# Optimization experiments

Hardware: AMD Instinct MI355X
Metric: run time of the kernel (lower is better)

## Reference

```python
import jax, jax.numpy as jnp
import numpy as np

D_MODEL = 1024
N_HEADS = 16
D_HEAD = 64
GROUP_SIZE = 2
N_GROUPS = N_HEADS // GROUP_SIZE


def setup_inputs() -> dict:
    key = jax.random.key(0)
    k1, k2, k3, k4, k5 = jax.random.split(key, 5)
    def xavier(k, shape):
        fan_in, fan_out = shape[0], int(np.prod(shape[1:]))
        bound = float(np.sqrt(6.0 / (fan_in + fan_out)))
        return jax.random.uniform(k, shape, jnp.float32, -bound, bound)
    return {
        'resid': jax.random.normal(k1, (2, 2048, D_MODEL), jnp.float32),
        'W_Q': xavier(k2, (D_MODEL, N_HEADS, D_HEAD)),
        'W_K': xavier(k3, (D_MODEL, N_GROUPS, D_HEAD)),
        'W_V': xavier(k4, (D_MODEL, N_GROUPS, D_HEAD)),
        'W_out': xavier(k5, (D_HEAD, N_HEADS, D_MODEL)),
        'b_out': jnp.zeros((D_MODEL,), jnp.float32),
    }


def reference(resid, W_Q, W_K, W_V, W_out, b_out):
    batch, seq, _ = resid.shape
    # q: [b, s, n_heads, d_head] -> [b, s, n_groups, group_size, d_head]
    q = jnp.einsum('bsd,dhe->bshe', resid, W_Q)
    q = q.reshape(batch, seq, N_GROUPS, GROUP_SIZE, D_HEAD)
    k = jnp.einsum('bsd,dge->bsge', resid, W_K)  # [b, s, g, e]
    v = jnp.einsum('bsd,dge->bsge', resid, W_V)
    # scores: [b, g, group_size, qseq, kseq]
    scores = jnp.einsum('bqgre,bkge->bgrqk', q, k) / jnp.sqrt(jnp.float32(D_HEAD))
    causal_mask = jnp.triu(jnp.ones((seq, seq), bool), k=1)
    scores = jnp.where(causal_mask, jnp.float32(-1000000.0), scores)
    probs = jax.nn.softmax(scores, axis=-1)
    # z: [b, q, g, r, e]
    z = jnp.einsum('bgrqk,bkge->bqgre', probs, v)
    z = z.reshape(batch, seq, N_HEADS, D_HEAD)
    out = jnp.einsum('bshe,ehd->bsd', z, W_out) + b_out
    return out
```

## Files before the change

### kernel.cpp

```cpp
#include <hip/hip_runtime.h>

#define BATCH   2
#define SEQ     2048
#define DMODEL  1024
#define NHEADS  16
#define DHEAD   64
#define NGROUPS 8
#define NTOK    (BATCH * SEQ)
#define QKV_N   2048

typedef unsigned short ushort_t;
typedef unsigned int u32;
typedef __attribute__((ext_vector_type(8))) short short8;
typedef __attribute__((ext_vector_type(4))) float f32x4;
typedef __attribute__((ext_vector_type(16))) float f32x16;

#define MFMA16(a, b, c) __builtin_amdgcn_mfma_f32_16x16x32_bf16((a), (b), (c), 0, 0, 0)
#define MFMA32(a, b, c) __builtin_amdgcn_mfma_f32_32x32x16_bf16((a), (b), (c), 0, 0, 0)

#define GLOAD16(gp, lp)                                                        \
    __builtin_amdgcn_global_load_lds(                                          \
        (const u32 __attribute__((address_space(1)))*)(gp),                    \
        (u32 __attribute__((address_space(3)))*)(lp), 16, 0, 0)

#define CVTPK(dst, lo, hi) \
    asm("v_cvt_pk_bf16_f32 %0, %1, %2" : "=v"(dst) : "v"(lo), "v"(hi))

#define PLSWAP(a, b) \
    asm("v_permlane32_swap_b32 %0, %1" : "+v"(a), "+v"(b))

__device__ __forceinline__ ushort_t f2bu(float x) {
    unsigned u = __builtin_bit_cast(unsigned, x);
    unsigned r = (u + 0x7fffu + ((u >> 16) & 1u)) >> 16;
    return (ushort_t)r;
}

__global__ __launch_bounds__(256) void prep(
    const float* __restrict__ resid,
    const float* __restrict__ Wq, const float* __restrict__ Wk,
    const float* __restrict__ Wv, const float* __restrict__ Wout,
    ushort_t* __restrict__ rbf, ushort_t* __restrict__ Wt,
    ushort_t* __restrict__ Wot)
{
    __shared__ float Ws[64][65];
    const int t = threadIdx.x;
    const int bid = blockIdx.x;

    if (bid < 4096) {
        const int i4 = bid * 256 + t;
        union { float4 v; float f[4]; } a;
        a.v = *reinterpret_cast<const float4*>(resid + (size_t)i4 * 4);
        union { uint2 v; ushort_t u[4]; } o;
        #pragma unroll
        for (int j = 0; j < 4; ++j) o.u[j] = f2bu(a.f[j]);
        *reinterpret_cast<uint2*>(rbf + (size_t)i4 * 4) = o.v;
        return;
    }

    if (bid < 4096 + 512) {
        const int rel = bid - 4096;
        const int k0 = (rel & 15) * 64;
        const int n0 = (rel >> 4) * 64;

        const float* src; int stride, boff;
        if (n0 < 1024)       { src = Wq; stride = 1024; boff = n0; }
        else if (n0 < 1536)  { src = Wk; stride = 512;  boff = n0 - 1024; }
        else                 { src = Wv; stride = 512;  boff = n0 - 1536; }

        #pragma unroll
        for (int i = 0; i < 4; ++i) {
            const int c = i * 256 + t;
            const int row = c >> 4, cc = (c & 15) * 4;
            union { float4 v; float f[4]; } a;
            a.v = *reinterpret_cast<const float4*>(
                src + (size_t)(k0 + row) * stride + boff + cc);
            #pragma unroll
            for (int j = 0; j < 4; ++j) Ws[row][cc + j] = a.f[j];
        }
        __syncthreads();
        #pragma unroll
        for (int i = 0; i < 2; ++i) {
            const int c = i * 256 + t;
            const int nr = c >> 3, kc = (c & 7) * 8;
            union { uint4 v; ushort_t u[8]; } o;
            #pragma unroll
            for (int j = 0; j < 8; ++j) o.u[j] = f2bu(Ws[kc + j][nr]);
            *reinterpret_cast<uint4*>(Wt + (size_t)(n0 + nr) * 1024 + k0 + kc) = o.v;
        }
        return;
    }

    {
        const int rel = bid - 4608;
        const int d0 = (rel & 15) * 64;
        const int h  = rel >> 4;

        #pragma unroll
        for (int i = 0; i < 4; ++i) {
            const int c = i * 256 + t;
            const int e = c >> 4, dd = (c & 15) * 4;
            union { float4 v; float f[4]; } a;
            a.v = *reinterpret_cast<const float4*>(
                Wout + (size_t)(e * 16 + h) * 1024 + d0 + dd);
            #pragma unroll
            for (int j = 0; j < 4; ++j) Ws[e][dd + j] = a.f[j];
        }
        __syncthreads();
        #pragma unroll
        for (int i = 0; i < 2; ++i) {
            const int c = i * 256 + t;
            const int dr = c >> 3, ec = (c & 7) * 8;
            union { uint4 v; ushort_t u[8]; } o;
            #pragma unroll
            for (int j = 0; j < 8; ++j) o.u[j] = f2bu(Ws[ec + j][dr]);
            *reinterpret_cast<uint4*>(Wot + (size_t)(d0 + dr) * 1024 + h * 64 + ec) = o.v;
        }
    }
}

__global__ __launch_bounds__(256) void tr_v(
    const ushort_t* __restrict__ qkv, ushort_t* __restrict__ Vt)
{
    __shared__ ushort_t T[64][72];
    const int t  = threadIdx.x;
    const int s0 = blockIdx.x * 64;
    const int g  = blockIdx.y;
    const int b  = blockIdx.z;

    #pragma unroll
    for (int i = 0; i < 2; ++i) {
        const int c = i * 256 + t;
        const int row = c >> 3, ec = (c & 7) * 8;
        *reinterpret_cast<uint4*>(&T[row][ec]) =
            *reinterpret_cast<const uint4*>(
                qkv + (size_t)(b * SEQ + s0 + row) * QKV_N + 1536 + g * 64 + ec);
    }
    __syncthreads();
    #pragma unroll
    for (int i = 0; i < 2; ++i) {
        const int c = i * 256 + t;
        const int er = c >> 3, sc = (c & 7) * 8;
        union { uint4 v; ushort_t u[8]; } o;
        #pragma unroll
        for (int j = 0; j < 8; ++j) o.u[j] = T[sc + j][er];
        *reinterpret_cast<uint4*>(
            Vt + (size_t)((b * NGROUPS + g) * 64 + er) * SEQ + s0 + sc) = o.v;
    }
}

__global__ __launch_bounds__(512) void qkv_gemm(
    const ushort_t* __restrict__ A, const ushort_t* __restrict__ Bt,
    ushort_t* __restrict__ C)
{
    __shared__ ushort_t As[2][128][64];
    __shared__ ushort_t Bs[2][128][64];

    const int t = threadIdx.x;
    const int wave = t >> 6, lane = t & 63;
    const int quad = lane >> 4, x = lane & 15;
    const int wm = (wave >> 1) * 32, wn = (wave & 1) * 64;
    const int m0 = blockIdx.y * 128, n0 = blockIdx.x * 128;

    const int sr8 = lane >> 3;
    const int gc  = (lane & 7) ^ sr8;

    f32x4 acc[2][4];
    #pragma unroll
    for (int i = 0; i < 2; ++i)
        #pragma unroll
        for (int j = 0; j < 4; ++j) acc[i][j] = (f32x4)(0.f);

    #pragma unroll
    for (int s = 0; s < 2; ++s) {
        const int r0 = (wave * 2 + s) * 8;
        GLOAD16(A  + (size_t)(m0 + r0 + sr8) * 1024 + gc * 8, &As[0][r0][0]);
        GLOAD16(Bt + (size_t)(n0 + r0 + sr8) * 1024 + gc * 8, &Bs[0][r0][0]);
    }
    __syncthreads();

    int cur = 0;
    for (int k0 = 0; k0 < 1024; k0 += 64) {
        if (k0 + 64 < 1024) {
            #pragma unroll
            for (int s = 0; s < 2; ++s) {
                const int r0 = (wave * 2 + s) * 8;
                GLOAD16(A  + (size_t)(m0 + r0 + sr8) * 1024 + k0 + 64 + gc * 8,
                        &As[cur ^ 1][r0][0]);
                GLOAD16(Bt + (size_t)(n0 + r0 + sr8) * 1024 + k0 + 64 + gc * 8,
                        &Bs[cur ^ 1][r0][0]);
            }
        }
        #pragma unroll
        for (int j = 0; j < 2; ++j) {
            const int cs = ((j * 4 + quad) ^ (x & 7)) * 8;
            short8 af[2], bf[4];
            #pragma unroll
            for (int mt = 0; mt < 2; ++mt)
                af[mt] = *reinterpret_cast<const short8*>(&As[cur][wm + mt * 16 + x][cs]);
            #pragma unroll
            for (int nt = 0; nt < 4; ++nt)
                bf[nt] = *reinterpret_cast<const short8*>(&Bs[cur][wn + nt * 16 + x][cs]);
            #pragma unroll
            for (int mt = 0; mt < 2; ++mt)
                #pragma unroll
                for (int nt = 0; nt < 4; ++nt)
                    acc[mt][nt] = MFMA16(af[mt], bf[nt], acc[mt][nt]);
        }
        __syncthreads();
        cur ^= 1;
    }

    #pragma unroll
    for (int mt = 0; mt < 2; ++mt)
        #pragma unroll
        for (int nt = 0; nt < 4; ++nt)
            #pragma unroll
            for (int r = 0; r < 4; ++r) {
                const int row = m0 + wm + mt * 16 + quad * 4 + r;
                const int col = n0 + wn + nt * 16 + x;
                C[(size_t)row * QKV_N + col] = f2bu(acc[mt][nt][r]);
            }
}

__global__ __launch_bounds__(512) void out_gemm(
    const ushort_t* __restrict__ A, const ushort_t* __restrict__ Bt,
    const float* __restrict__ bias, float* __restrict__ C)
{
    __shared__ ushort_t As[2][128][64];
    __shared__ ushort_t Bs[2][64][64];

    const int t = threadIdx.x;
    const int wave = t >> 6, lane = t & 63;
    const int quad = lane >> 4, x = lane & 15;
    const int wm = (wave >> 1) * 32, wn = (wave & 1) * 32;
    const int m0 = blockIdx.y * 128, n0 = blockIdx.x * 64;

    const int sr8 = lane >> 3;
    const int gc  = (lane & 7) ^ sr8;

    f32x4 acc[2][2];
    #pragma unroll
    for (int i = 0; i < 2; ++i)
        #pragma unroll
        for (int j = 0; j < 2; ++j) acc[i][j] = (f32x4)(0.f);

    #pragma unroll
    for (int s = 0; s < 2; ++s) {
        const int r0 = (wave * 2 + s) * 8;
        GLOAD16(A + (size_t)(m0 + r0 + sr8) * 1024 + gc * 8, &As[0][r0][0]);
    }
    {
        const int r0 = wave * 8;
        GLOAD16(Bt + (size_t)(n0 + r0 + sr8) * 1024 + gc * 8, &Bs[0][r0][0]);
    }
    __syncthreads();

    int cur = 0;
    for (int k0 = 0; k0 < 1024; k0 += 64) {
        if (k0 + 64 < 1024) {
            #pragma unroll
            for (int s = 0; s < 2; ++s) {
                const int r0 = (wave * 2 + s) * 8;
                GLOAD16(A + (size_t)(m0 + r0 + sr8) * 1024 + k0 + 64 + gc * 8,
                        &As[cur ^ 1][r0][0]);
            }
            const int r0 = wave * 8;
            GLOAD16(Bt + (size_t)(n0 + r0 + sr8) * 1024 + k0 + 64 + gc * 8,
                    &Bs[cur ^ 1][r0][0]);
        }
        #pragma unroll
        for (int j = 0; j < 2; ++j) {
            const int cs = ((j * 4 + quad) ^ (x & 7)) * 8;
            short8 af[2], bf[2];
            #pragma unroll
            for (int mt = 0; mt < 2; ++mt)
                af[mt] = *reinterpret_cast<const short8*>(&As[cur][wm + mt * 16 + x][cs]);
            #pragma unroll
            for (int nt = 0; nt < 2; ++nt)
                bf[nt] = *reinterpret_cast<const short8*>(&Bs[cur][wn + nt * 16 + x][cs]);
            #pragma unroll
            for (int mt = 0; mt < 2; ++mt)
                #pragma unroll
                for (int nt = 0; nt < 2; ++nt)
                    acc[mt][nt] = MFMA16(af[mt], bf[nt], acc[mt][nt]);
        }
        __syncthreads();
        cur ^= 1;
    }

    float bv[2];
    #pragma unroll
    for (int nt = 0; nt < 2; ++nt) bv[nt] = bias[n0 + wn + nt * 16 + x];

    #pragma unroll
    for (int mt = 0; mt < 2; ++mt)
        #pragma unroll
        for (int nt = 0; nt < 2; ++nt)
            #pragma unroll
            for (int r = 0; r < 4; ++r) {
                const int row = m0 + wm + mt * 16 + quad * 4 + r;
                const int col = n0 + wn + nt * 16 + x;
                C[(size_t)row * 1024 + col] = acc[mt][nt][r] + bv[nt];
            }
}

__global__ __launch_bounds__(512, 4) void attn(
    const ushort_t* __restrict__ qkv, const ushort_t* __restrict__ Vt,
    ushort_t* __restrict__ z)
{
    __shared__ float Ob1[64 * 64];
    __shared__ float Ob3[64 * 64];
    __shared__ float Ofin[64 * 64];
    __shared__ float Lb1[64];
    __shared__ float Lb3[64];

    const int t = threadIdx.x;
    const int wave = t >> 6, lane = t & 63;
    const int x31 = lane & 31, hi = lane >> 5;
    const int rw = wave & 1;
    const int kw = wave >> 1;

    const int h  = blockIdx.x;
    const int qp = blockIdx.y;
    const int b  = blockIdx.z;
    const int g  = h >> 1;

    const ushort_t* kg = qkv + (size_t)(b * SEQ) * QKV_N + 1024 + g * 64;
    const ushort_t* vg = Vt + (size_t)((b * NGROUPS + g) * 64) * SEQ;

    const int qloc = rw * 32 + x31;

    #pragma unroll
    for (int phase = 0; phase < 2; ++phase) {
        const int qt = phase ? (31 - qp) : qp;
        const int qrow0 = qt * 64;
        const int nkt = (qt >> 1) + 1;

        short8 aq[4];
        #pragma unroll
        for (int sl = 0; sl < 4; ++sl)
            aq[sl] = *reinterpret_cast<const short8*>(
                qkv + (size_t)(b * SEQ + qrow0 + qloc) * QKV_N + h * 64 + sl * 16 + hi * 8);

        f32x16 o0 = (f32x16)(0.f), o1 = (f32x16)(0.f);
        float lown = 0.f;

        for (int kt = 0; kt < nkt; ++kt) {
            const int cbase = kt * 128 + kw * 32;
            const int qmin  = qrow0 + rw * 32;
            if (cbase > qmin + 31) continue;
            const bool full = (cbase + 31 <= qmin);

            short8 kf[4];
            #pragma unroll
            for (int sl = 0; sl < 4; ++sl)
                kf[sl] = *reinterpret_cast<const short8*>(
                    kg + (size_t)(cbase + x31) * QKV_N + sl * 16 + hi * 8);

            short8 vf0[2], vf1[2];
            #pragma unroll
            for (int ks = 0; ks < 2; ++ks) {
                const size_t vcol = (size_t)(kt * 128 + (kw * 4 + ks * 2 + hi) * 8);
                vf0[ks] = *reinterpret_cast<const short8*>(
                    vg + (size_t)x31 * SEQ + vcol);
                vf1[ks] = *reinterpret_cast<const short8*>(
                    vg + (size_t)(32 + x31) * SEQ + vcol);
            }

            f32x16 st = (f32x16)(0.f);
            __builtin_amdgcn_s_setprio(1);
            #pragma unroll
            for (int sl = 0; sl < 4; ++sl)
                st = MFMA32(kf[sl], aq[sl], st);
            __builtin_amdgcn_s_setprio(0);

            const int ql = qmin + x31 - cbase;
            float p[16];
            float s16 = 0.f;
            #pragma unroll
            for (int r = 0; r < 16; ++r) {
                const int keyoff = (r & 3) + 8 * (r >> 2);
                float pv = __expf(st[r] * 0.125f);
                if (!full) pv = (keyoff + 4 * hi > ql) ? 0.f : pv;
                p[r] = pv;
                s16 += pv;
            }
            lown += s16;

            u32 pk0, pk1, pk2, pk3, pk4, pk5, pk6, pk7;
            CVTPK(pk0, p[0],  p[1]);  CVTPK(pk1, p[2],  p[3]);
            CVTPK(pk2, p[4],  p[5]);  CVTPK(pk3, p[6],  p[7]);
            CVTPK(pk4, p[8],  p[9]);  CVTPK(pk5, p[10], p[11]);
            CVTPK(pk6, p[12], p[13]); CVTPK(pk7, p[14], p[15]);
            PLSWAP(pk0, pk2); PLSWAP(pk1, pk3);
            PLSWAP(pk4, pk6); PLSWAP(pk5, pk7);
            union { u32 u[4]; short8 s; } f0, f1;
            f0.u[0] = pk0; f0.u[1] = pk1; f0.u[2] = pk2; f0.u[3] = pk3;
            f1.u[0] = pk4; f1.u[1] = pk5; f1.u[2] = pk6; f1.u[3] = pk7;

            __builtin_amdgcn_s_setprio(1);
            #pragma unroll
            for (int ks = 0; ks < 2; ++ks) {
                const short8 pf = ks ? f1.s : f0.s;
                o0 = MFMA32(vf0[ks], pf, o0);
                o1 = MFMA32(vf1[ks], pf, o1);
            }
            __builtin_amdgcn_s_setprio(0);
        }

        float ltot;
        {
            u32 la = __builtin_bit_cast(u32, lown), lb = la;
            PLSWAP(la, lb);
            const float lpart = __builtin_bit_cast(float, hi ? la : lb);
            ltot = lown + lpart;
        }

        if (kw == 1 || kw == 3) {
            float* Obx = (kw == 1) ? Ob1 : Ob3;
            float* Lbx = (kw == 1) ? Lb1 : Lb3;
            #pragma unroll
            for (int r = 0; r < 16; ++r) {
                const int e = (r & 3) + 8 * (r >> 2) + 4 * hi;
                Obx[e * 64 + qloc]        = o0[r];
                Obx[(32 + e) * 64 + qloc] = o1[r];
            }
            if (hi == 0) Lbx[qloc] = ltot;
        }
        __syncthreads();
        if (kw == 0 || kw == 2) {
            const float* Obx = (kw == 0) ? Ob1 : Ob3;
            const float* Lbx = (kw == 0) ? Lb1 : Lb3;
            #pragma unroll
            for (int r = 0; r < 16; ++r) {
                const int e = (r & 3) + 8 * (r >> 2) + 4 * hi;
                o0[r] += Obx[e * 64 + qloc];
                o1[r] += Obx[(32 + e) * 64 + qloc];
            }
            ltot += Lbx[qloc];
        }
        __syncthreads();
        if (kw == 2) {
            #pragma unroll
            for (int r = 0; r < 16; ++r) {
                const int e = (r & 3) + 8 * (r >> 2) + 4 * hi;
                Ob1[e * 64 + qloc]        = o0[r];
                Ob1[(32 + e) * 64 + qloc] = o1[r];
            }
            if (hi == 0) Lb1[qloc] = ltot;
        }
        __syncthreads();
        if (kw == 0) {
            #pragma unroll
            for (int r = 0; r < 16; ++r) {
                const int e = (r & 3) + 8 * (r >> 2) + 4 * hi;
                o0[r] += Ob1[e * 64 + qloc];
                o1[r] += Ob1[(32 + e) * 64 + qloc];
            }
            ltot += Lb1[qloc];
            const float inv = 1.f / ltot;
            #pragma unroll
            for (int r = 0; r < 16; ++r) {
                const int e = (r & 3) + 8 * (r >> 2) + 4 * hi;
                Ofin[e * 64 + qloc]        = o0[r] * inv;
                Ofin[(32 + e) * 64 + qloc] = o1[r] * inv;
            }
        }
        __syncthreads();

        {
            const int q = t >> 3, ec = t & 7;
            union { u32 u[4]; uint4 v; } pkz;
            #pragma unroll
            for (int j2 = 0; j2 < 4; ++j2) {
                float v0 = Ofin[(ec * 8 + 2 * j2) * 64 + q];
                float v1 = Ofin[(ec * 8 + 2 * j2 + 1) * 64 + q];
                CVTPK(pkz.u[j2], v0, v1);
            }
            *reinterpret_cast<uint4*>(
                z + (size_t)(b * SEQ + qrow0 + q) * 1024 + h * 64 + ec * 8) = pkz.v;
        }
    }
}

extern "C" void kernel_launch(void* const* d_in, const int* in_sizes, int n_in,
                              void* d_out, int out_size, void* d_ws, size_t ws_size,
                              hipStream_t stream)
{
    const float* resid = (const float*)d_in[0];
    const float* Wq    = (const float*)d_in[1];
    const float* Wk    = (const float*)d_in[2];
    const float* Wv    = (const float*)d_in[3];
    const float* Wout  = (const float*)d_in[4];
    const float* bout  = (const float*)d_in[5];
    float* out = (float*)d_out;

    ushort_t* rbf   = (ushort_t*)d_ws;
    ushort_t* wqkvt = rbf   + (size_t)NTOK * DMODEL;
    ushort_t* woutt = wqkvt + (size_t)QKV_N * DMODEL;
    ushort_t* qkv   = woutt + (size_t)DMODEL * DMODEL;
    ushort_t* z     = qkv   + (size_t)NTOK * QKV_N;
    ushort_t* vt    = rbf;

    prep     <<<dim3(4864), 256, 0, stream>>>(resid, Wq, Wk, Wv, Wout,
                                              rbf, wqkvt, woutt);
    qkv_gemm <<<dim3(16, 32), 512, 0, stream>>>(rbf, wqkvt, qkv);
    tr_v     <<<dim3(SEQ / 64, NGROUPS, BATCH), 256, 0, stream>>>(qkv, vt);
    attn     <<<dim3(16, 16, 2), 512, 0, stream>>>(qkv, vt, z);
    out_gemm <<<dim3(16, 32), 512, 0, stream>>>(z, woutt, bout, out);
}
```

Before: 199.3 us.

## Prefetch next K tile in attention loop and swizzle GEMM block order

The attention inner loop is unrolled by two with ping-pong K register buffers, so the next key tile is loaded while the current tile's MFMAs and softmax run. Each wave's trip count is computed up front instead of skipping tiles with continue. Both GEMMs remap block indices with a swizzle to change L2 reuse across concurrently running blocks. A trailing __syncthreads is added between phases, and the extra registers could reduce occupancy.

```diff
diff --git a/kernel.cpp b/kernel.cpp
--- a/kernel.cpp
+++ b/kernel.cpp
@@ -159,7 +159,10 @@
     const int wave = t >> 6, lane = t & 63;
     const int quad = lane >> 4, x = lane & 15;
     const int wm = (wave >> 1) * 32, wn = (wave & 1) * 64;
-    const int m0 = blockIdx.y * 128, n0 = blockIdx.x * 128;
+
+    const int lin = blockIdx.x + 16 * blockIdx.y;
+    const int swz = ((lin & 7) << 6) | (lin >> 3);
+    const int m0 = (swz >> 4) * 128, n0 = (swz & 15) * 128;
 
     const int sr8 = lane >> 3;
     const int gc  = (lane & 7) ^ sr8;
@@ -233,7 +236,10 @@
     const int wave = t >> 6, lane = t & 63;
     const int quad = lane >> 4, x = lane & 15;
     const int wm = (wave >> 1) * 32, wn = (wave & 1) * 32;
-    const int m0 = blockIdx.y * 128, n0 = blockIdx.x * 64;
+
+    const int lin = blockIdx.x + 16 * blockIdx.y;
+    const int swz = ((lin & 7) << 6) | (lin >> 3);
+    const int m0 = (swz >> 4) * 128, n0 = (swz & 15) * 64;
 
     const int sr8 = lane >> 3;
     const int gc  = (lane & 7) ^ sr8;
@@ -303,6 +309,72 @@
                 C[(size_t)row * 1024 + col] = acc[mt][nt][r] + bv[nt];
             }
 }
+
+#define LOADK(KT, DST)                                                        \
+    {                                                                         \
+        const int cb_ = (KT) * 128 + kw * 32;                                 \
+        _Pragma("unroll")                                                     \
+        for (int sl = 0; sl < 4; ++sl)                                        \
+            DST[sl] = *reinterpret_cast<const short8*>(                       \
+                kg + (size_t)(cb_ + x31) * QKV_N + sl * 16 + hi * 8);         \
+    }
+
+#define ATTN_ITER(KT, KF, KNEXT)                                              \
+    {                                                                         \
+        const int kt_ = (KT);                                                 \
+        const int cbase_ = kt_ * 128 + kw * 32;                               \
+        const bool full_ = (cbase_ + 31 <= qmin);                             \
+                               \
+        short8 vf0_[2], vf1_[2];                                              \
+        _Pragma("unroll")                                                     \
+        for (int ks = 0; ks < 2; ++ks) {                                      \
+            const size_t vcol_ =                                              \
+                (size_t)(kt_ * 128 + (kw * 4 + ks * 2 + hi) * 8);             \
+            vf0_[ks] = *reinterpret_cast<const short8*>(                      \
+                vg + (size_t)x31 * SEQ + vcol_);                              \
+            vf1_[ks] = *reinterpret_cast<const short8*>(                      \
+                vg + (size_t)(32 + x31) * SEQ + vcol_);                       \
+        }                                                                     \
+                                            \
+        if (kt_ + 1 < nkt_w) LOADK(kt_ + 1, KNEXT);                           \
+                                                           \
+        f32x16 st = (f32x16)(0.f);                                            \
+        __builtin_amdgcn_s_setprio(1);                                        \
+        _Pragma("unroll")                                                     \
+        for (int sl = 0; sl < 4; ++sl) st = MFMA32(KF[sl], aq[sl], st);       \
+        __builtin_amdgcn_s_setprio(0);                                        \
+                                                     \
+        const int ql_ = qmin + x31 - cbase_;                                  \
+        float p[16];                                                          \
+        float s16 = 0.f;                                                      \
+        _Pragma("unroll")                                                     \
+        for (int r = 0; r < 16; ++r) {                                        \
+            const int keyoff = (r & 3) + 8 * (r >> 2);                        \
+            float pv = __expf(st[r] * 0.125f);                                \
+            if (!full_) pv = (keyoff + 4 * hi > ql_) ? 0.f : pv;              \
+            p[r] = pv;                                                        \
+            s16 += pv;                                                        \
+        }                                                                     \
+        lown += s16;                                                          \
+                                         \
+        u32 pk0, pk1, pk2, pk3, pk4, pk5, pk6, pk7;                           \
+        CVTPK(pk0, p[0],  p[1]);  CVTPK(pk1, p[2],  p[3]);                    \
+        CVTPK(pk2, p[4],  p[5]);  CVTPK(pk3, p[6],  p[7]);                    \
+        CVTPK(pk4, p[8],  p[9]);  CVTPK(pk5, p[10], p[11]);                   \
+        CVTPK(pk6, p[12], p[13]); CVTPK(pk7, p[14], p[15]);                   \
+        PLSWAP(pk0, pk2); PLSWAP(pk1, pk3);                                   \
+        PLSWAP(pk4, pk6); PLSWAP(pk5, pk7);                                   \
+        union { u32 u[4]; short8 s; } f0, f1;                                 \
+        f0.u[0] = pk0; f0.u[1] = pk1; f0.u[2] = pk2; f0.u[3] = pk3;           \
+        f1.u[0] = pk4; f1.u[1] = pk5; f1.u[2] = pk6; f1.u[3] = pk7;           \
+                                                        \
+        __builtin_amdgcn_s_setprio(1);                                        \
+        o0 = MFMA32(vf0_[0], f0.s, o0);                                       \
+        o1 = MFMA32(vf1_[0], f0.s, o1);                                       \
+        o0 = MFMA32(vf0_[1], f1.s, o0);                                       \
+        o1 = MFMA32(vf1_[1], f1.s, o1);                                       \
+        __builtin_amdgcn_s_setprio(0);                                        \
+    }
 
 __global__ __launch_bounds__(512, 4) void attn(
     const ushort_t* __restrict__ qkv, const ushort_t* __restrict__ Vt,
@@ -335,6 +407,14 @@
         const int qt = phase ? (31 - qp) : qp;
         const int qrow0 = qt * 64;
         const int nkt = (qt >> 1) + 1;
+        const int qmin = qrow0 + rw * 32;
+
+        int nkt_w;
+        {
+            const int d = qmin + 31 - kw * 32;
+            nkt_w = (d < 0) ? 0 : (d / 128) + 1;
+            if (nkt_w > nkt) nkt_w = nkt;
+        }
 
         short8 aq[4];
         #pragma unroll
@@ -345,67 +425,13 @@
         f32x16 o0 = (f32x16)(0.f), o1 = (f32x16)(0.f);
         float lown = 0.f;
 
-        for (int kt = 0; kt < nkt; ++kt) {
-            const int cbase = kt * 128 + kw * 32;
-            const int qmin  = qrow0 + rw * 32;
-            if (cbase > qmin + 31) continue;
-            const bool full = (cbase + 31 <= qmin);
-
-            short8 kf[4];
-            #pragma unroll
-            for (int sl = 0; sl < 4; ++sl)
-                kf[sl] = *reinterpret_cast<const short8*>(
-                    kg + (size_t)(cbase + x31) * QKV_N + sl * 16 + hi * 8);
-
-            short8 vf0[2], vf1[2];
-            #pragma unroll
-            for (int ks = 0; ks < 2; ++ks) {
-                const size_t vcol = (size_t)(kt * 128 + (kw * 4 + ks * 2 + hi) * 8);
-                vf0[ks] = *reinterpret_cast<const short8*>(
-                    vg + (size_t)x31 * SEQ + vcol);
-                vf1[ks] = *reinterpret_cast<const short8*>(
-                    vg + (size_t)(32 + x31) * SEQ + vcol);
-            }
-
-            f32x16 st = (f32x16)(0.f);
-            __builtin_amdgcn_s_setprio(1);
-            #pragma unroll
-            for (int sl = 0; sl < 4; ++sl)
-                st = MFMA32(kf[sl], aq[sl], st);
-            __builtin_amdgcn_s_setprio(0);
-
-            const int ql = qmin + x31 - cbase;
-            float p[16];
-            float s16 = 0.f;
-            #pragma unroll
-            for (int r = 0; r < 16; ++r) {
-                const int keyoff = (r & 3) + 8 * (r >> 2);
-                float pv = __expf(st[r] * 0.125f);
-                if (!full) pv = (keyoff + 4 * hi > ql) ? 0.f : pv;
-                p[r] = pv;
-                s16 += pv;
-            }
-            lown += s16;
-
-            u32 pk0, pk1, pk2, pk3, pk4, pk5, pk6, pk7;
-            CVTPK(pk0, p[0],  p[1]);  CVTPK(pk1, p[2],  p[3]);
-            CVTPK(pk2, p[4],  p[5]);  CVTPK(pk3, p[6],  p[7]);
-            CVTPK(pk4, p[8],  p[9]);  CVTPK(pk5, p[10], p[11]);
-            CVTPK(pk6, p[12], p[13]); CVTPK(pk7, p[14], p[15]);
-            PLSWAP(pk0, pk2); PLSWAP(pk1, pk3);
-            PLSWAP(pk4, pk6); PLSWAP(pk5, pk7);
-            union { u32 u[4]; short8 s; } f0, f1;
-            f0.u[0] = pk0; f0.u[1] = pk1; f0.u[2] = pk2; f0.u[3] = pk3;
-            f1.u[0] = pk4; f1.u[1] = pk5; f1.u[2] = pk6; f1.u[3] = pk7;
-
-            __builtin_amdgcn_s_setprio(1);
-            #pragma unroll
-            for (int ks = 0; ks < 2; ++ks) {
-                const short8 pf = ks ? f1.s : f0.s;
-                o0 = MFMA32(vf0[ks], pf, o0);
-                o1 = MFMA32(vf1[ks], pf, o1);
-            }
-            __builtin_amdgcn_s_setprio(0);
+        short8 kA[4], kB[4];
+        if (nkt_w > 0) {
+            LOADK(0, kA);
+            for (int kt2 = 0; kt2 < nkt_w; kt2 += 2) {
+                ATTN_ITER(kt2, kA, kB);
+                if (kt2 + 1 < nkt_w) ATTN_ITER(kt2 + 1, kB, kA);
+            }
         }
 
         float ltot;
@@ -480,6 +506,7 @@
             *reinterpret_cast<uint4*>(
                 z + (size_t)(b * SEQ + qrow0 + q) * 1024 + h * 64 + ec * 8) = pkz.v;
         }
+        __syncthreads();
     }
 }
 
```

Result: slower. 220.4 us (+10.6%).
